# Kernel tuning notes

Hardware: AMD Instinct MI355X
Metric: run time of the kernel (lower is better)

The kernel has to match this reference:

```python
import jax, jax.numpy as jnp
import numpy as np

Q = 128      # number of slices
S = 8        # slice_length = C // Q = 1024 // 128
H = 32       # unit_dim[0]
BN_EPS = 1e-3  # Keras BatchNormalization default epsilon


def setup_inputs() -> dict:
    key = jax.random.key(0)
    ks = jax.random.split(key, 5)
    B = 32768
    x = jax.random.normal(ks[0], (B, 1, 1, Q * S), dtype=jnp.float32)
    # Per-slice (grouped) parameters for the q=128 independent MLPs.
    W1 = jax.random.normal(ks[1], (Q, S, H), dtype=jnp.float32) / np.sqrt(S)
    b1 = jnp.zeros((Q, H), dtype=jnp.float32)
    gamma = jnp.ones((Q, H), dtype=jnp.float32)
    beta = jnp.zeros((Q, H), dtype=jnp.float32)
    mov_mean = 0.1 * jax.random.normal(ks[2], (Q, H), dtype=jnp.float32)
    mov_var = jnp.ones((Q, H), dtype=jnp.float32) + 0.1 * jax.random.uniform(ks[3], (Q, H), dtype=jnp.float32)
    W2 = jax.random.normal(ks[4], (Q, H, 1), dtype=jnp.float32) / np.sqrt(H)
    b2 = jnp.zeros((Q, 1), dtype=jnp.float32)
    return {"x": x, "W1": W1, "b1": b1, "gamma": gamma, "beta": beta,
            "mov_mean": mov_mean, "mov_var": mov_var, "W2": W2, "b2": b2}


def reference(x, W1, b1, gamma, beta, mov_mean, mov_var, W2, b2):
    B = x.shape[0]
    xs = x.reshape(B, Q, -1)                       # (B, Q, S)
    # Grouped Dense(32) + ELU, all 128 slices in one batched matmul
    h = jnp.einsum('bqs,qsh->bqh', xs, W1) + b1    # (B, Q, H)
    h = jax.nn.elu(h)
    # BatchNormalization (inference: moving statistics)
    inv = gamma * jax.lax.rsqrt(mov_var + BN_EPS)  # (Q, H)
    h = (h - mov_mean) * inv + beta
    # Grouped Dense(1)
    out = jnp.einsum('bqh,qho->bqo', h, W2) + b2   # (B, Q, 1)
    return out[..., 0]                              # (B, Q)
```

## Files before the change

### kernel.cpp

```cpp
#include <hip/hip_runtime.h>
#include <hip/hip_bf16.h>


#define QN 128
#define SN 8
#define HN 32
#define XROW 1024
#define BN_EPS 1e-3f
#define ROWS_BLK 128
#define QBLK 16

typedef short bf16x8 __attribute__((ext_vector_type(8)));
typedef float f32x16 __attribute__((ext_vector_type(16)));
typedef unsigned int u32;

typedef __attribute__((address_space(1))) void as1_void;
typedef __attribute__((address_space(3))) void as3_void;

#define WS_A_BYTES (QN * 64 * 16)
#define WS_C_OFF   WS_A_BYTES
#define WS_C_BYTES (QN * 32 * 4)
#define WS_W_OFF   (WS_C_OFF + WS_C_BYTES)
#define WS_W_BYTES (QN * 32 * 4)
#define WS_B2_OFF  (WS_W_OFF + WS_W_BYTES)

static __device__ __forceinline__ u32 pkbf(float lo, float hi) {
    union { __hip_bfloat162 h2; u32 u; } c;
    c.h2 = __float22bfloat162_rn(float2{lo, hi});
    return c.u;
}

__global__ void divenc_prep(const float* __restrict__ W1, const float* __restrict__ b1,
                            const float* __restrict__ gamma_, const float* __restrict__ beta_,
                            const float* __restrict__ mmean, const float* __restrict__ mvar,
                            const float* __restrict__ W2, const float* __restrict__ b2,
                            unsigned char* __restrict__ ws)
{
    const int q = blockIdx.x;
    const int m = threadIdx.x;

    u32 d0 = 0, d1 = 0, d2 = 0, d3 = 0;
    if (m < 32) {
        d0 = pkbf(W1[(q*SN + 0)*HN + m], W1[(q*SN + 1)*HN + m]);
        d1 = pkbf(W1[(q*SN + 2)*HN + m], W1[(q*SN + 3)*HN + m]);
        d2 = pkbf(W1[(q*SN + 4)*HN + m], W1[(q*SN + 5)*HN + m]);
        d3 = pkbf(W1[(q*SN + 6)*HN + m], W1[(q*SN + 7)*HN + m]);
    }
    ((uint4*)ws)[q*64 + m] = uint4{d0, d1, d2, d3};

    float* wsC  = (float*)(ws + WS_C_OFF);
    float* wsW  = (float*)(ws + WS_W_OFF);
    float* wsB2 = (float*)(ws + WS_B2_OFF);
    if (m < 32) {
        const int half = m >> 4, r = m & 15;
        const int h = (r & 3) + 8*(r >> 2) + 4*half;
        wsC[q*32 + m] = b1[q*HN + h];
        float inv = gamma_[q*HN+h] * rsqrtf(mvar[q*HN+h] + BN_EPS);
        wsW[q*32 + m] = inv * W2[q*HN + h];
    }
    if (m == 0) {
        float acc = b2[q];
        for (int h = 0; h < HN; ++h) {
            float inv = gamma_[q*HN+h] * rsqrtf(mvar[q*HN+h] + BN_EPS);
            acc += (beta_[q*HN+h] - mmean[q*HN+h]*inv) * W2[q*HN+h];
        }
        wsB2[q] = acc;
    }
}

__device__ __forceinline__
void stage_chunk(const float* __restrict__ x, u32* lds_base,
                 int b0, int q0, int c, int wv, int lane)
{
    #pragma unroll
    for (int k = 0; k < 2; ++k) {
        const int i  = wv * 2 + k;
        const int r  = i * 2 + (lane >> 5);
        const int jl = (lane & 31) ^ r;
        const float* src = x + (size_t)(b0 + c * 32 + r) * XROW + q0 * SN + jl * 4;
        u32* dst = lds_base + i * 256;
        __builtin_amdgcn_global_load_lds((const as1_void*)src, (as3_void*)dst, 16, 0, 0);
    }
}

__global__ __launch_bounds__(512, 4)
void divenc_mfma(const float* __restrict__ x, const unsigned char* __restrict__ ws,
                 float* __restrict__ out)
{
    const int lane = threadIdx.x & 63;
    const int wv   = threadIdx.x >> 6;
    const int half = lane >> 5;
    const int rr   = lane & 31;
    const int b0   = blockIdx.x * ROWS_BLK;
    const int q0   = blockIdx.y * QBLK;

    const uint4* wsA  = (const uint4*)ws;
    const float* wsC  = (const float*)(ws + WS_C_OFF);
    const float* wsW  = (const float*)(ws + WS_W_OFF);
    const float* wsB2 = (const float*)(ws + WS_B2_OFF);

    __shared__ u32   xbuf[2][32 * 128];
    __shared__ float slab[32][17];

    stage_chunk(x, xbuf[0], b0, q0, 0, wv, lane);

    #pragma unroll 1
    for (int c = 0; c < 4; ++c) {
        __syncthreads();

        if (c < 3) stage_chunk(x, xbuf[(c + 1) & 1], b0, q0, c + 1, wv, lane);

        const u32* xb = xbuf[c & 1];
        #pragma unroll
        for (int qg = 0; qg < 2; ++qg) {
            const int ql = qg * 8 + wv;
            const int q  = q0 + ql;

            union { uint4 u; bf16x8 v; } A;
            A.u = wsA[q * 64 + lane];

            f32x16 cini;
            const float* cp_ = wsC + q * 32 + half * 16;
            #pragma unroll
            for (int r = 0; r < 16; ++r) cini[r] = cp_[r];
            float w2r[16];
            const float* wp_ = wsW + q * 32 + half * 16;
            #pragma unroll
            for (int r = 0; r < 16; ++r) w2r[r] = wp_[r];
            const float b2p = wsB2[q];

            const u32* rowp = xb + rr * 128;
            const uint4 xw0 = *(const uint4*)(rowp + ((2 * ql)     ^ rr) * 4);
            const uint4 xw1 = *(const uint4*)(rowp + ((2 * ql + 1) ^ rr) * 4);

            union { uint4 u; bf16x8 v; } B;
            B.u = uint4{ pkbf(__uint_as_float(xw0.x), __uint_as_float(xw0.y)),
                         pkbf(__uint_as_float(xw0.z), __uint_as_float(xw0.w)),
                         pkbf(__uint_as_float(xw1.x), __uint_as_float(xw1.y)),
                         pkbf(__uint_as_float(xw1.z), __uint_as_float(xw1.w)) };

            f32x16 D = __builtin_amdgcn_mfma_f32_32x32x16_bf16(A.v, B.v, cini, 0, 0, 0);

            float p = 0.f;
            #pragma unroll
            for (int r = 0; r < 16; ++r) {
                float z = D[r];
                float e = __expf(fminf(z, 0.f)) - 1.f;
                p = fmaf(fmaxf(z, e), w2r[r], p);
            }
            p += __shfl_xor(p, 32);
            if (half == 0) slab[rr][ql] = p + b2p;
        }

        __syncthreads();

        if (threadIdx.x < 128) {
            const int row = threadIdx.x >> 2;
            const int c4  = (threadIdx.x & 3) * 4;
            float4 vv;
            vv.x = slab[row][c4 + 0];
            vv.y = slab[row][c4 + 1];
            vv.z = slab[row][c4 + 2];
            vv.w = slab[row][c4 + 3];
            *(float4*)(out + (size_t)(b0 + c * 32 + row) * QN + q0 + c4) = vv;
        }
    }
}

extern "C" void kernel_launch(void* const* d_in, const int* in_sizes, int n_in,
                              void* d_out, int out_size, void* d_ws, size_t ws_size,
                              hipStream_t stream) {
    const float* x      = (const float*)d_in[0];
    const float* W1     = (const float*)d_in[1];
    const float* b1     = (const float*)d_in[2];
    const float* gamma_ = (const float*)d_in[3];
    const float* beta_  = (const float*)d_in[4];
    const float* mmean  = (const float*)d_in[5];
    const float* mvar   = (const float*)d_in[6];
    const float* W2     = (const float*)d_in[7];
    const float* b2     = (const float*)d_in[8];
    float* out = (float*)d_out;
    unsigned char* ws = (unsigned char*)d_ws;

    const int Btot = in_sizes[0] / XROW;

    divenc_prep<<<QN, 64, 0, stream>>>(W1, b1, gamma_, beta_, mmean, mvar, W2, b2, ws);
    divenc_mfma<<<dim3(Btot / ROWS_BLK, QN / QBLK), 512, 0, stream>>>(x, ws, out);
}
```

Baseline: 61.58 us.

## Fold b1 into MFMA via ones column, split ELU sum, batch output writes

The layer-1 bias b1 now rides in the MFMA's K dimension: the upper lanes of B carry a bf16 1.0 and the A workspace holds b1, so the per-q 16-float accumulator init load goes away. The ELU is rewritten as exp(min(z,0)) plus relu(z) with two separate dot products, and the constant -1 term is folded into the precomputed b2. The per-chunk second barrier and small store are replaced by one slab for all 128 rows, written out once at the end by all threads. Launch bounds rise to 8 waves per SIMD target. The bias is now rounded to bf16, which adds a small precision risk.

```diff
diff --git a/kernel.cpp b/kernel.cpp
--- a/kernel.cpp
+++ b/kernel.cpp
@@ -8,6 +8,7 @@
 #define XROW 1024
 #define BN_EPS 1e-3f
 #define ROWS_BLK 128
+#define CHUNK 32
 #define QBLK 16
 
 typedef short bf16x8 __attribute__((ext_vector_type(8)));
@@ -18,9 +19,7 @@
 typedef __attribute__((address_space(3))) void as3_void;
 
 #define WS_A_BYTES (QN * 64 * 16)
-#define WS_C_OFF   WS_A_BYTES
-#define WS_C_BYTES (QN * 32 * 4)
-#define WS_W_OFF   (WS_C_OFF + WS_C_BYTES)
+#define WS_W_OFF   WS_A_BYTES
 #define WS_W_BYTES (QN * 32 * 4)
 #define WS_B2_OFF  (WS_W_OFF + WS_W_BYTES)
 
@@ -45,16 +44,16 @@
         d1 = pkbf(W1[(q*SN + 2)*HN + m], W1[(q*SN + 3)*HN + m]);
         d2 = pkbf(W1[(q*SN + 4)*HN + m], W1[(q*SN + 5)*HN + m]);
         d3 = pkbf(W1[(q*SN + 6)*HN + m], W1[(q*SN + 7)*HN + m]);
+    } else {
+        d0 = pkbf(b1[q*HN + (m - 32)], 0.f);
     }
     ((uint4*)ws)[q*64 + m] = uint4{d0, d1, d2, d3};
 
-    float* wsC  = (float*)(ws + WS_C_OFF);
     float* wsW  = (float*)(ws + WS_W_OFF);
     float* wsB2 = (float*)(ws + WS_B2_OFF);
     if (m < 32) {
         const int half = m >> 4, r = m & 15;
         const int h = (r & 3) + 8*(r >> 2) + 4*half;
-        wsC[q*32 + m] = b1[q*HN + h];
         float inv = gamma_[q*HN+h] * rsqrtf(mvar[q*HN+h] + BN_EPS);
         wsW[q*32 + m] = inv * W2[q*HN + h];
     }
@@ -62,14 +61,15 @@
         float acc = b2[q];
         for (int h = 0; h < HN; ++h) {
             float inv = gamma_[q*HN+h] * rsqrtf(mvar[q*HN+h] + BN_EPS);
-            acc += (beta_[q*HN+h] - mmean[q*HN+h]*inv) * W2[q*HN+h];
+            float w2p = inv * W2[q*HN + h];
+            acc += (beta_[q*HN+h] - mmean[q*HN+h]*inv) * W2[q*HN+h] - w2p;
         }
         wsB2[q] = acc;
     }
 }
 
 __device__ __forceinline__
-void stage_chunk(const float* __restrict__ x, u32* lds_base,
+void stage_chunk(const float* __restrict__ x, u32* buf,
                  int b0, int q0, int c, int wv, int lane)
 {
     #pragma unroll
@@ -77,30 +77,31 @@
         const int i  = wv * 2 + k;
         const int r  = i * 2 + (lane >> 5);
         const int jl = (lane & 31) ^ r;
-        const float* src = x + (size_t)(b0 + c * 32 + r) * XROW + q0 * SN + jl * 4;
-        u32* dst = lds_base + i * 256;
+        const float* src = x + (size_t)(b0 + c * CHUNK + r) * XROW + q0 * SN + jl * 4;
+        u32* dst = buf + i * 256;
         __builtin_amdgcn_global_load_lds((const as1_void*)src, (as3_void*)dst, 16, 0, 0);
     }
 }
 
-__global__ __launch_bounds__(512, 4)
+__global__ __launch_bounds__(512, 8)
 void divenc_mfma(const float* __restrict__ x, const unsigned char* __restrict__ ws,
                  float* __restrict__ out)
 {
-    const int lane = threadIdx.x & 63;
-    const int wv   = threadIdx.x >> 6;
+    const int tid  = threadIdx.x;
+    const int lane = tid & 63;
+    const int wv   = tid >> 6;
     const int half = lane >> 5;
-    const int rr   = lane & 31;
+    const int bl   = lane & 31;
+    const bool hi  = lane >= 32;
     const int b0   = blockIdx.x * ROWS_BLK;
     const int q0   = blockIdx.y * QBLK;
 
     const uint4* wsA  = (const uint4*)ws;
-    const float* wsC  = (const float*)(ws + WS_C_OFF);
     const float* wsW  = (const float*)(ws + WS_W_OFF);
     const float* wsB2 = (const float*)(ws + WS_B2_OFF);
 
-    __shared__ u32   xbuf[2][32 * 128];
-    __shared__ float slab[32][17];
+    __shared__ u32   xbuf[2][CHUNK * 128];
+    __shared__ float slab[ROWS_BLK][QBLK + 1];
 
     stage_chunk(x, xbuf[0], b0, q0, 0, wv, lane);
 
@@ -111,59 +112,62 @@
         if (c < 3) stage_chunk(x, xbuf[(c + 1) & 1], b0, q0, c + 1, wv, lane);
 
         const u32* xb = xbuf[c & 1];
+
         #pragma unroll
         for (int qg = 0; qg < 2; ++qg) {
-            const int ql = qg * 8 + wv;
-            const int q  = q0 + ql;
+            const int qloc = qg * 8 + wv;
+            const int q    = q0 + qloc;
 
             union { uint4 u; bf16x8 v; } A;
             A.u = wsA[q * 64 + lane];
 
-            f32x16 cini;
-            const float* cp_ = wsC + q * 32 + half * 16;
-            #pragma unroll
-            for (int r = 0; r < 16; ++r) cini[r] = cp_[r];
             float w2r[16];
             const float* wp_ = wsW + q * 32 + half * 16;
             #pragma unroll
             for (int r = 0; r < 16; ++r) w2r[r] = wp_[r];
             const float b2p = wsB2[q];
 
-            const u32* rowp = xb + rr * 128;
-            const uint4 xw0 = *(const uint4*)(rowp + ((2 * ql)     ^ rr) * 4);
-            const uint4 xw1 = *(const uint4*)(rowp + ((2 * ql + 1) ^ rr) * 4);
+            const u32* rowp = xb + bl * 128;
+            const uint4 xw0 = *(const uint4*)(rowp + (((2 * qloc)     ^ bl) * 4));
+            const uint4 xw1 = *(const uint4*)(rowp + (((2 * qloc + 1) ^ bl) * 4));
 
             union { uint4 u; bf16x8 v; } B;
-            B.u = uint4{ pkbf(__uint_as_float(xw0.x), __uint_as_float(xw0.y)),
-                         pkbf(__uint_as_float(xw0.z), __uint_as_float(xw0.w)),
-                         pkbf(__uint_as_float(xw1.x), __uint_as_float(xw1.y)),
-                         pkbf(__uint_as_float(xw1.z), __uint_as_float(xw1.w)) };
+            B.u = uint4{
+                hi ? 0x00003F80u : pkbf(__uint_as_float(xw0.x), __uint_as_float(xw0.y)),
+                hi ? 0u          : pkbf(__uint_as_float(xw0.z), __uint_as_float(xw0.w)),
+                hi ? 0u          : pkbf(__uint_as_float(xw1.x), __uint_as_float(xw1.y)),
+                hi ? 0u          : pkbf(__uint_as_float(xw1.z), __uint_as_float(xw1.w)) };
 
-            f32x16 D = __builtin_amdgcn_mfma_f32_32x32x16_bf16(A.v, B.v, cini, 0, 0, 0);
+            const f32x16 Z = {0.f,0.f,0.f,0.f,0.f,0.f,0.f,0.f,
+                              0.f,0.f,0.f,0.f,0.f,0.f,0.f,0.f};
+            f32x16 D = __builtin_amdgcn_mfma_f32_32x32x16_bf16(A.v, B.v, Z, 0, 0, 0);
 
-            float p = 0.f;
+            float p0 = 0.f, p1 = 0.f;
             #pragma unroll
             for (int r = 0; r < 16; ++r) {
-                float z = D[r];
-                float e = __expf(fminf(z, 0.f)) - 1.f;
-                p = fmaf(fmaxf(z, e), w2r[r], p);
+                const float z = D[r];
+                const float E = __expf(fminf(z, 0.f));
+                const float R = fmaxf(z, 0.f);
+                p0 = fmaf(E, w2r[r], p0);
+                p1 = fmaf(R, w2r[r], p1);
             }
+            float p = p0 + p1;
             p += __shfl_xor(p, 32);
-            if (half == 0) slab[rr][ql] = p + b2p;
+            if (!hi) slab[c * CHUNK + bl][qloc] = p + b2p;
         }
+    }
 
-        __syncthreads();
+    __syncthreads();
 
-        if (threadIdx.x < 128) {
-            const int row = threadIdx.x >> 2;
-            const int c4  = (threadIdx.x & 3) * 4;
-            float4 vv;
-            vv.x = slab[row][c4 + 0];
-            vv.y = slab[row][c4 + 1];
-            vv.z = slab[row][c4 + 2];
-            vv.w = slab[row][c4 + 3];
-            *(float4*)(out + (size_t)(b0 + c * 32 + row) * QN + q0 + c4) = vv;
-        }
+    {
+        const int row = tid >> 2;
+        const int c4  = (tid & 3) * 4;
+        float4 vv;
+        vv.x = slab[row][c4 + 0];
+        vv.y = slab[row][c4 + 1];
+        vv.z = slab[row][c4 + 2];
+        vv.w = slab[row][c4 + 3];
+        *(float4*)(out + (size_t)(b0 + row) * QN + q0 + c4) = vv;
     }
 }
 
```

Result: faster. 53.63 us (-12.9%).
